# Performance work log

Hardware: AMD Instinct MI355X
Metric: run time of the kernel (lower is better)

## Reference

```python
import jax, jax.numpy as jnp
import numpy as np

K = 50          # NEC paper uses p=50 neighbors
DELTA = 1e-3    # kernel smoothing constant


def setup_inputs() -> dict:
    key = jax.random.key(0)
    ks = jax.random.split(key, 8)
    B, D_IN, D, A, C = 512, 2, 128, 3, 200000
    s = lambda fan_in: 1.0 / np.sqrt(fan_in)
    return {
        "x": jax.random.normal(ks[0], (B, D_IN), jnp.float32),
        "W1": jax.random.normal(ks[1], (D_IN, D), jnp.float32) * s(D_IN),
        "b1": jnp.zeros((D,), jnp.float32),
        "W2": jax.random.normal(ks[2], (D, D), jnp.float32) * s(D),
        "b2": jnp.zeros((D,), jnp.float32),
        "W3": jax.random.normal(ks[3], (D, D), jnp.float32) * s(D),
        "b3": jnp.zeros((D,), jnp.float32),
        "W4": jax.random.normal(ks[4], (D, D), jnp.float32) * s(D),
        "b4": jnp.zeros((D,), jnp.float32),
        "keys": jax.random.normal(ks[5], (A, C, D), jnp.float32),
        "mem_values": jax.random.normal(ks[6], (A, C), jnp.float32),
    }


def _encode(x, W1, b1, W2, b2, W3, b3, W4, b4):
    h = jax.nn.relu(x @ W1 + b1)
    h = jax.nn.relu(h @ W2 + b2)
    h = jax.nn.relu(h @ W3 + b3)
    return h @ W4 + b4  # [B, D]


def _dnd_lookup(h, keys, mem_values):
    # h: [B, D]; keys: [A, C, D]; mem_values: [A, C]
    q2 = jnp.sum(h * h, axis=-1)                       # [B]
    k2 = jnp.sum(keys * keys, axis=-1)                 # [A, C]
    cross = jnp.einsum("bd,acd->bac", h, keys)         # [B, A, C]
    d2 = jnp.maximum(q2[:, None, None] + k2[None] - 2.0 * cross, 0.0)
    neg_d, idx = jax.lax.top_k(-d2, K)                  # [B, A, K]
    d_top = -neg_d
    w = 1.0 / (d_top + DELTA)                           # NEC kernel
    w = w / jnp.sum(w, axis=-1, keepdims=True)
    a_idx = jnp.arange(keys.shape[0])[None, :, None]    # [1, A, 1]
    v_top = mem_values[a_idx, idx]                      # gather -> [B, A, K]
    values = jnp.sum(w * v_top, axis=-1)                # [B, A]
    return values


def reference(x, W1, b1, W2, b2, W3, b3, W4, b4, keys, mem_values):
    h = _encode(x, W1, b1, W2, b2, W3, b3, W4, b4)
    values = _dnd_lookup(h, keys, mem_values)
    actions = jnp.argmax(values, axis=-1)
    return values, actions
```

## Files before the change

kernel.cpp:

```cpp
#include <hip/hip_runtime.h>
#include <hip/hip_bf16.h>
#include <math.h>

#define B_    512
#define DIM   128
#define A_    3
#define C_    200000
#define K_    50
#define DELTA 1e-3

typedef __attribute__((ext_vector_type(8))) short bf16x8;
typedef __attribute__((ext_vector_type(4))) float f32x4;

#define NBIN_A 128
#define CAP_A  1024
#define ROWCH  12500

#define NBLK4  250
#define GT4    32
#define GTPB4  25

#define AOFF_H64   0u
#define AOFF_H32   524288u
#define AOFF_HBF   786432u
#define AOFF_Q2    917504u
#define AOFF_V64   1718272u
#define AOFF_BINS  8022016u
#define NEED_A     (8022016ull + 307200000ull)

#define NBIN_B 192
#define CAP_B  768
#define BM_B   64
#define BN_B   128
#define TPC_B  16
#define CHUNK_B (TPC_B*BN_B)
#define NCH_B  ((C_ + CHUNK_B - 1)/CHUNK_B)

#define BOFF_H32   0u
#define BOFF_H64   262144u
#define BOFF_Q2    786432u
#define BOFF_K2    788480u
#define BOFF_HIST  3188480u
#define BOFF_TAU   4368128u
#define BOFF_CNT   4374272u
#define BOFF_V64   4380416u
#define BOFF_CAND  4392704u

static __device__ inline unsigned short f2bf(float x) {
    union { float f; unsigned u; } c; c.f = x;
    unsigned r = (c.u + 0x7FFFu + ((c.u >> 16) & 1u)) >> 16;
    return (unsigned short)r;
}
static __device__ inline unsigned pkbf(float a, float b) {
    __hip_bfloat162 t = __float22bfloat162_rn(make_float2(a, b));
    union { __hip_bfloat162 h; unsigned u; } cv; cv.h = t; return cv.u;
}

__global__ __launch_bounds__(128) void mlp_kernel(
    const float* __restrict__ x,
    const float* __restrict__ W1, const float* __restrict__ b1,
    const float* __restrict__ W2, const float* __restrict__ b2,
    const float* __restrict__ W3, const float* __restrict__ b3,
    const float* __restrict__ W4, const float* __restrict__ b4,
    float* __restrict__ h32, unsigned short* __restrict__ hbf,
    double* __restrict__ h64, float* __restrict__ q2)
{
    int b = blockIdx.x, t = threadIdx.x;
    __shared__ double s0[DIM], s1[DIM];
    double x0 = (double)x[b*2+0], x1 = (double)x[b*2+1];
    double h = x0*(double)W1[t] + x1*(double)W1[DIM+t] + (double)b1[t];
    s0[t] = h > 0.0 ? h : 0.0;
    __syncthreads();
    double acc = (double)b2[t];
    for (int k = 0; k < DIM; k++) acc += s0[k]*(double)W2[k*DIM+t];
    s1[t] = acc > 0.0 ? acc : 0.0;
    __syncthreads();
    acc = (double)b3[t];
    for (int k = 0; k < DIM; k++) acc += s1[k]*(double)W3[k*DIM+t];
    s0[t] = acc > 0.0 ? acc : 0.0;
    __syncthreads();
    acc = (double)b4[t];
    for (int k = 0; k < DIM; k++) acc += s0[k]*(double)W4[k*DIM+t];
    h64[b*DIM+t] = acc;
    float hf = (float)acc;
    h32[b*DIM+t] = hf;
    hbf[b*DIM+t] = f2bf(hf);
    s1[t] = acc*acc;
    __syncthreads();
    for (int s = 64; s > 0; s >>= 1) { if (t < s) s1[t] += s1[t+s]; __syncthreads(); }
    if (t == 0) q2[b] = (float)s1[0];
}

static __device__ inline void load2(float4 lv[2], const float* __restrict__ ka,
                                    int nrow, int hh) {
    const float4* gp = (const float4*)(ka + (size_t)nrow*DIM) + hh*2;
    lv[0] = gp[0]; lv[1] = gp[1];
}
static __device__ inline void conv_store32(const float4 lv[2], char* sBn,
                                           float* k2n, int r, int hh) {
    float4 v0 = lv[0], v1 = lv[1];
    float ss = v0.x*v0.x + v0.y*v0.y + v0.z*v0.z + v0.w*v0.w
             + v1.x*v1.x + v1.y*v1.y + v1.z*v1.z + v1.w*v1.w;
    int4 pk;
    pk.x = (int)pkbf(v0.x, v0.y); pk.y = (int)pkbf(v0.z, v0.w);
    pk.z = (int)pkbf(v1.x, v1.y); pk.w = (int)pkbf(v1.z, v1.w);
    *(int4*)(sBn + r*256 + ((hh ^ (r & 7)) << 4)) = pk;
    ss += __shfl_xor(ss, 1, 64);
    ss += __shfl_xor(ss, 2, 64);
    ss += __shfl_xor(ss, 4, 64);
    ss += __shfl_xor(ss, 8, 64);
    if (hh == 0) k2n[r] = ss;
}

__global__ __launch_bounds__(512, 1) void gemm4_kernel(
    const float* __restrict__ keys, const unsigned short* __restrict__ hbf,
    const float* __restrict__ q2, unsigned char* __restrict__ bins)
{
    const int blk = blockIdx.x, a = blockIdx.y;
    const int tid = threadIdx.x;
    const int lane = tid & 63, w = tid >> 6;
    const int lm = lane & 15, kh = lane >> 4;

    __shared__ __align__(16) short sA[512*128];
    __shared__ __align__(16) short sB[2][32*128];
    __shared__ float q2s[512];
    __shared__ float k2s[2][32];

    #pragma unroll
    for (int u = 0; u < 16; u++) {
        int idx = u*512 + tid;
        int rr = idx >> 4, cc = idx & 15;
        int4 gv = ((const int4*)hbf)[rr*16 + cc];
        *(int4*)((char*)sA + rr*256 + ((cc ^ (rr & 7)) << 4)) = gv;
    }
    q2s[tid] = q2[tid];

    const int r = tid >> 4, hh = tid & 15;
    const float* ka = keys + (size_t)a*C_*DIM;
    const int nbase = blk*(GT4*GTPB4);

    float4 lv[2];
    load2(lv, ka, nbase + r, hh);
    conv_store32(lv, (char*)&sB[0][0], k2s[0], r, hh);
    __syncthreads();

    unsigned char* rp0; unsigned char* rp1; unsigned char* rp2; unsigned char* rp3;
    {
        unsigned char* base = bins + (size_t)(a*B_)*C_ + kh*4;
        rp0 = base + (size_t)(w*64 +  0 + lm)*C_;
        rp1 = base + (size_t)(w*64 + 16 + lm)*C_;
        rp2 = base + (size_t)(w*64 + 32 + lm)*C_;
        rp3 = base + (size_t)(w*64 + 48 + lm)*C_;
    }

    unsigned pkp[8];
    #pragma unroll
    for (int u = 0; u < 8; u++) pkp[u] = 0;
    int n0_prev = 0;

    int cur = 0;
    for (int t = 0; t < GTPB4; t++) {
        const int n0 = nbase + t*GT4;
        const bool more = (t + 1 < GTPB4);

        if (more) load2(lv, ka, n0 + GT4 + r, hh);
        if (t > 0) {
            *(unsigned*)(rp0 + n0_prev     ) = pkp[0];
            *(unsigned*)(rp0 + n0_prev + 16) = pkp[1];
            *(unsigned*)(rp1 + n0_prev     ) = pkp[2];
            *(unsigned*)(rp1 + n0_prev + 16) = pkp[3];
            *(unsigned*)(rp2 + n0_prev     ) = pkp[4];
            *(unsigned*)(rp2 + n0_prev + 16) = pkp[5];
            *(unsigned*)(rp3 + n0_prev     ) = pkp[6];
            *(unsigned*)(rp3 + n0_prev + 16) = pkp[7];
        }

        f32x4 acc[2][4];
        #pragma unroll
        for (int i = 0; i < 2; i++)
            #pragma unroll
            for (int j = 0; j < 4; j++) acc[i][j] = (f32x4){0.f, 0.f, 0.f, 0.f};

        const char* sBc = (const char*)&sB[cur][0];
        #pragma unroll
        for (int kst = 0; kst < 4; kst++) {
            bf16x8 af[2], bfv[4];
            #pragma unroll
            for (int i = 0; i < 2; i++) {
                int nr = i*16 + lm;
                af[i] = *(const bf16x8*)(sBc + nr*256 + ((((kst<<2) + kh) ^ (nr & 7)) << 4));
            }
            #pragma unroll
            for (int j = 0; j < 4; j++) {
                int br = w*64 + j*16 + lm;
                bfv[j] = *(const bf16x8*)((const char*)sA + br*256 + ((((kst<<2) + kh) ^ (br & 7)) << 4));
            }
            #pragma unroll
            for (int i = 0; i < 2; i++)
                #pragma unroll
                for (int j = 0; j < 4; j++)
                    acc[i][j] = __builtin_amdgcn_mfma_f32_16x16x32_bf16(af[i], bfv[j], acc[i][j], 0, 0, 0);
        }

        {
            float4 kq0 = *(const float4*)&k2s[cur][kh*4];
            float4 kq1 = *(const float4*)&k2s[cur][16 + kh*4];
            #pragma unroll
            for (int j = 0; j < 4; j++) {
                float q2v = q2s[w*64 + j*16 + lm];
                #pragma unroll
                for (int i = 0; i < 2; i++) {
                    float4 kq = (i == 0) ? kq0 : kq1;
                    unsigned pk = 0;
                    #pragma unroll
                    for (int rg = 0; rg < 4; rg++) {
                        float kv = (rg == 0) ? kq.x : (rg == 1) ? kq.y : (rg == 2) ? kq.z : kq.w;
                        float d2v = (q2v + kv) - 2.0f*acc[i][j][rg];
                        float dc = fminf(fmaxf(d2v, 16.0f), 4095.0f);
                        unsigned bin = (__float_as_uint(dc) >> 19) - 2096u;
                        pk |= bin << (8*rg);
                    }
                    pkp[j*2 + i] = pk;
                }
            }
            n0_prev = n0;
        }

        if (more) conv_store32(lv, (char*)&sB[cur ^ 1][0], k2s[cur ^ 1], r, hh);
        __syncthreads();
        cur ^= 1;
    }
    *(unsigned*)(rp0 + n0_prev     ) = pkp[0];
    *(unsigned*)(rp0 + n0_prev + 16) = pkp[1];
    *(unsigned*)(rp1 + n0_prev     ) = pkp[2];
    *(unsigned*)(rp1 + n0_prev + 16) = pkp[3];
    *(unsigned*)(rp2 + n0_prev     ) = pkp[4];
    *(unsigned*)(rp2 + n0_prev + 16) = pkp[5];
    *(unsigned*)(rp3 + n0_prev     ) = pkp[6];
    *(unsigned*)(rp3 + n0_prev + 16) = pkp[7];
}

__global__ __launch_bounds__(512) void finish_kernel(
    const unsigned char* __restrict__ bins, const float* __restrict__ keys,
    const double* __restrict__ h64, const float* __restrict__ mem_values,
    float* __restrict__ out_values, double* __restrict__ val64)
{
    const int q = blockIdx.x;
    const int a = q >> 9, b = q & 511;
    const int p = b*A_ + a;
    const int tid = threadIdx.x;

    __shared__ unsigned hist_s[NBIN_A*32];
    __shared__ unsigned hc[NBIN_A];
    __shared__ double hd[DIM];
    __shared__ unsigned char minb[ROWCH + 12];
    __shared__ int    cidx[CAP_A];
    __shared__ double d2s[CAP_A];
    __shared__ float  vs[CAP_A];
    __shared__ double redv[8];
    __shared__ int    redi8[8];
    __shared__ double acc_w, acc_wv;
    __shared__ unsigned cnt_s;
    __shared__ int thr_s;

    for (int i = tid; i < NBIN_A*32; i += 512) hist_s[i] = 0;
    for (int i = tid; i < DIM; i += 512) hd[i] = h64[(size_t)b*DIM + i];
    if (tid == 0) { cnt_s = 0; acc_w = 0.0; acc_wv = 0.0; }
    __syncthreads();

    const uint4* row = (const uint4*)(bins + (size_t)q*C_);
    const int rep = tid & 31;

    auto proc1 = [&](uint4 v, int ch) {
        unsigned d[4] = {v.x, v.y, v.z, v.w};
        unsigned mn = 255u;
        #pragma unroll
        for (int e = 0; e < 4; e++) {
            unsigned x = d[e];
            unsigned b0 =  x        & 127u;
            unsigned b1 = (x >>  8) & 127u;
            unsigned b2 = (x >> 16) & 127u;
            unsigned b3 = (x >> 24) & 127u;
            atomicAdd(&hist_s[b0*32 + rep], 1u);
            atomicAdd(&hist_s[b1*32 + rep], 1u);
            atomicAdd(&hist_s[b2*32 + rep], 1u);
            atomicAdd(&hist_s[b3*32 + rep], 1u);
            unsigned m01 = b0 < b1 ? b0 : b1;
            unsigned m23 = b2 < b3 ? b2 : b3;
            unsigned m = m01 < m23 ? m01 : m23;
            mn = m < mn ? m : mn;
        }
        minb[ch] = (unsigned char)mn;
    };

    {
        uint4 va[4], vb[4];
        #pragma unroll
        for (int u = 0; u < 4; u++) va[u] = row[u*512 + tid];
        #pragma unroll
        for (int g = 0; g < 6; g += 2) {
            #pragma unroll
            for (int u = 0; u < 4; u++) vb[u] = row[((g+1)*4 + u)*512 + tid];
            #pragma unroll
            for (int u = 0; u < 4; u++) proc1(va[u], (g*4 + u)*512 + tid);
            if (g + 2 < 6) {
                #pragma unroll
                for (int u = 0; u < 4; u++) va[u] = row[((g+2)*4 + u)*512 + tid];
            }
            #pragma unroll
            for (int u = 0; u < 4; u++) proc1(vb[u], ((g+1)*4 + u)*512 + tid);
        }
        if (tid < ROWCH - 24*512) {
            int ch = 24*512 + tid;
            proc1(row[ch], ch);
        }
    }
    __syncthreads();
    if (tid < NBIN_A) {
        unsigned s = 0;
        #pragma unroll
        for (int r2 = 0; r2 < 32; r2++) s += hist_s[tid*32 + r2];
        hc[tid] = s;
    }
    __syncthreads();
    if (tid == 0) {
        unsigned cum = 0; int jsel = NBIN_A-1;
        for (int j = 0; j < NBIN_A; j++) { cum += hc[j]; if (cum >= K_) { jsel = j; break; } }
        unsigned c1 = cum + (jsel+1 < NBIN_A ? hc[jsel+1] : 0u);
        unsigned c2 = c1  + (jsel+2 < NBIN_A ? hc[jsel+2] : 0u);
        int jt = (c2 <= 768u) ? jsel+2 : jsel+1;
        if (jt > NBIN_A-1) jt = NBIN_A-1;
        thr_s = jt + 1;
    }
    __syncthreads();
    const unsigned thr  = (unsigned)thr_s;
    const unsigned addv = (128u - thr) * 0x01010101u;
    for (int ch = tid; ch < ROWCH; ch += 512) {
        if ((unsigned)minb[ch] < thr) {
            uint4 v = row[ch];
            unsigned d[4] = {v.x, v.y, v.z, v.w};
            #pragma unroll
            for (int e = 0; e < 4; e++) {
                unsigned m = (d[e] + addv) & 0x80808080u;
                if (m != 0x80808080u) {
                    #pragma unroll
                    for (int by = 0; by < 4; by++) {
                        if (!((m >> (8*by + 7)) & 1u)) {
                            unsigned pos = atomicAdd(&cnt_s, 1u);
                            if (pos < CAP_A) cidx[pos] = ch*16 + e*4 + by;
                        }
                    }
                }
            }
        }
    }
    __syncthreads();
    int n = (int)cnt_s; if (n > CAP_A) n = CAP_A;

    for (int i = tid; i < n; i += 512) {
        int c = cidx[i];
        const float4* kr = (const float4*)(keys + ((size_t)a*C_ + c)*DIM);
        double s0 = 0.0, s1 = 0.0;
        #pragma unroll 4
        for (int kq = 0; kq < 32; kq++) {
            float4 kv = kr[kq];
            double d0 = hd[4*kq+0] - (double)kv.x;
            double d1 = hd[4*kq+1] - (double)kv.y;
            double d2 = hd[4*kq+2] - (double)kv.z;
            double d3 = hd[4*kq+3] - (double)kv.w;
            s0 += d0*d0 + d1*d1; s1 += d2*d2 + d3*d3;
        }
        d2s[i] = s0 + s1;
        vs[i]  = mem_values[(size_t)a*C_ + c];
    }
    __syncthreads();

    int kk = n < K_ ? n : K_;
    for (int t = 0; t < kk; t++) {
        double best = 1e300; int bi = -1;
        for (int i = tid; i < n; i += 512)
            if (d2s[i] < best) { best = d2s[i]; bi = i; }
        #pragma unroll
        for (int off = 32; off > 0; off >>= 1) {
            double ov = __shfl_xor(best, off, 64);
            int    oi = __shfl_xor(bi,   off, 64);
            if (ov < best) { best = ov; bi = oi; }
        }
        int wv = tid >> 6;
        if ((tid & 63) == 0) { redv[wv] = best; redi8[wv] = bi; }
        __syncthreads();
        if (tid == 0) {
            double bv = redv[0]; int wi = redi8[0];
            #pragma unroll
            for (int u = 1; u < 8; u++)
                if (redv[u] < bv) { bv = redv[u]; wi = redi8[u]; }
            double d = d2s[wi]; if (d < 0.0) d = 0.0;
            double wgt = 1.0 / (d + DELTA);
            acc_w += wgt; acc_wv += wgt * (double)vs[wi];
            d2s[wi] = 2e300;
        }
        __syncthreads();
    }
    if (tid == 0) {
        double v = acc_wv / acc_w;
        out_values[p] = (float)v;
        val64[p] = v;
    }
}

__global__ __launch_bounds__(256) void k2_kernel(const float* __restrict__ keys,
                                                 float* __restrict__ k2)
{
    int r = blockIdx.x*4 + (threadIdx.x >> 6);
    int lane = threadIdx.x & 63;
    float2 v = ((const float2*)keys)[(size_t)r*64 + lane];
    float s = v.x*v.x + v.y*v.y;
    #pragma unroll
    for (int off = 32; off > 0; off >>= 1) s += __shfl_down(s, off, 64);
    if (lane == 0) k2[r] = s;
}

template<int MODE>
__global__ __launch_bounds__(256) void pass_kernel(
    const float* __restrict__ keys, const float* __restrict__ h32,
    const float* __restrict__ q2,   const float* __restrict__ k2,
    unsigned* __restrict__ hist,    const float* __restrict__ tau,
    unsigned* __restrict__ cnt,     int* __restrict__ cand)
{
    const int bt = blockIdx.x;
    const int ch = blockIdx.y;
    const int a  = blockIdx.z;
    const int b0 = bt*BM_B;
    const int tid = threadIdx.x;
    const int tx = tid & 31, ty = tid >> 5;

    __shared__ float4 hs4[BM_B*33];
    __shared__ float4 ks4[BN_B*33];
    __shared__ float  q2s[BM_B];
    __shared__ float  taus[BM_B];
    __shared__ unsigned hist_s[MODE == 0 ? BM_B*NBIN_B : 1];

    #pragma unroll
    for (int q = 0; q < BM_B*32/256; q++) {
        int flat = q*256 + tid; int row = flat >> 5, kq = flat & 31;
        hs4[row*33 + kq] = ((const float4*)h32)[(size_t)(b0+row)*32 + kq];
    }
    if (tid < BM_B) {
        q2s[tid] = q2[b0+tid];
        if (MODE == 1) taus[tid] = tau[(b0+tid)*A_ + a];
    }
    if (MODE == 0) for (int i = tid; i < BM_B*NBIN_B; i += 256) hist_s[i] = 0;
    const float* __restrict__ k2g = k2 + (size_t)a*C_;

    for (int t = 0; t < TPC_B; t++) {
        int n0 = ch*CHUNK_B + t*BN_B;
        if (n0 >= C_) break;
        __syncthreads();
        #pragma unroll
        for (int q = 0; q < 16; q++) {
            int flat = q*256 + tid; int row = flat >> 5, kq = flat & 31;
            int nr = n0 + row; if (nr >= C_) nr = C_-1;
            ks4[row*33 + kq] = ((const float4*)keys)[((size_t)a*C_ + nr)*32 + kq];
        }
        __syncthreads();

        float acc[8][4];
        #pragma unroll
        for (int i = 0; i < 8; i++)
            #pragma unroll
            for (int j = 0; j < 4; j++) acc[i][j] = 0.0f;

        for (int kq = 0; kq < 32; kq++) {
            float4 hv[8], kv[4];
            #pragma unroll
            for (int i = 0; i < 8; i++) hv[i] = hs4[(ty*8+i)*33 + kq];
            #pragma unroll
            for (int j = 0; j < 4; j++) kv[j] = ks4[(j*32+tx)*33 + kq];
            #pragma unroll
            for (int i = 0; i < 8; i++)
                #pragma unroll
                for (int j = 0; j < 4; j++)
                    acc[i][j] += hv[i].x*kv[j].x + hv[i].y*kv[j].y
                               + hv[i].z*kv[j].z + hv[i].w*kv[j].w;
        }

        #pragma unroll
        for (int i = 0; i < 8; i++) {
            int bl = ty*8 + i;
            float q2b = q2s[bl];
            #pragma unroll
            for (int j = 0; j < 4; j++) {
                int n = n0 + j*32 + tx;
                if (n < C_) {
                    float d2f = fmaxf(q2b + k2g[n] - 2.0f*acc[i][j], 0.0f);
                    if (MODE == 0) {
                        int bin = (int)(__float_as_uint(d2f + 1.0f) >> 19) - 2032;
                        bin = bin < 0 ? 0 : (bin > NBIN_B-1 ? NBIN_B-1 : bin);
                        atomicAdd(&hist_s[bl*NBIN_B + bin], 1u);
                    } else {
                        if (d2f < taus[bl]) {
                            int p = (b0+bl)*A_ + a;
                            unsigned pos = atomicAdd(&cnt[p], 1u);
                            if (pos < CAP_B) cand[(size_t)p*CAP_B + pos] = n;
                        }
                    }
                }
            }
        }
    }
    if (MODE == 0) {
        __syncthreads();
        for (int i = tid; i < BM_B*NBIN_B; i += 256) {
            unsigned v = hist_s[i];
            if (v) {
                int bl = i / NBIN_B, bin = i % NBIN_B;
                atomicAdd(&hist[(size_t)((b0+bl)*A_ + a)*NBIN_B + bin], v);
            }
        }
    }
}

__global__ __launch_bounds__(256) void tauB_kernel(const unsigned* __restrict__ hist,
                                                   float* __restrict__ tau)
{
    int p = blockIdx.x*256 + threadIdx.x;
    if (p >= B_*A_) return;
    const unsigned* hp = hist + (size_t)p*NBIN_B;
    unsigned cum = 0; int jsel = NBIN_B-1;
    for (int j = 0; j < NBIN_B; j++) { cum += hp[j]; if (cum >= K_) { jsel = j; break; } }
    tau[p] = __uint_as_float((unsigned)(2034 + jsel) << 19) - 1.0f;
}

__global__ __launch_bounds__(256) void select_kernel(
    const float* __restrict__ keys, const double* __restrict__ h64,
    const float* __restrict__ mem_values,
    const unsigned* __restrict__ cnt, const int* __restrict__ cand,
    float* __restrict__ out_values, double* __restrict__ val64, int cap)
{
    int p = blockIdx.x; int b = p / A_, a = p % A_;
    int tid = threadIdx.x;
    __shared__ double hd[DIM];
    __shared__ double d2s[CAP_A];
    __shared__ float  vs[CAP_A];
    __shared__ double redv[4];
    __shared__ int    redi4[4];
    __shared__ double acc_w, acc_wv;

    for (int i = tid; i < DIM; i += 256) hd[i] = h64[(size_t)b*DIM + i];
    if (tid == 0) { acc_w = 0.0; acc_wv = 0.0; }
    __syncthreads();

    int n = (int)cnt[p]; if (n > cap) n = cap;
    for (int i = tid; i < n; i += 256) {
        int c = cand[(size_t)p*cap + i];
        const float4* kr = (const float4*)(keys + ((size_t)a*C_ + c)*DIM);
        double s0 = 0.0, s1 = 0.0;
        #pragma unroll 4
        for (int kq = 0; kq < 32; kq++) {
            float4 kv = kr[kq];
            double d0 = hd[4*kq+0] - (double)kv.x;
            double d1 = hd[4*kq+1] - (double)kv.y;
            double d2 = hd[4*kq+2] - (double)kv.z;
            double d3 = hd[4*kq+3] - (double)kv.w;
            s0 += d0*d0 + d1*d1; s1 += d2*d2 + d3*d3;
        }
        d2s[i] = s0 + s1;
        vs[i]  = mem_values[(size_t)a*C_ + c];
    }
    __syncthreads();

    int kk = n < K_ ? n : K_;
    for (int t = 0; t < kk; t++) {
        double best = 1e300; int bi = -1;
        for (int i = tid; i < n; i += 256)
            if (d2s[i] < best) { best = d2s[i]; bi = i; }
        #pragma unroll
        for (int off = 32; off > 0; off >>= 1) {
            double ov = __shfl_xor(best, off, 64);
            int    oi = __shfl_xor(bi,   off, 64);
            if (ov < best) { best = ov; bi = oi; }
        }
        int wv = tid >> 6;
        if ((tid & 63) == 0) { redv[wv] = best; redi4[wv] = bi; }
        __syncthreads();
        if (tid == 0) {
            double bv = redv[0]; int wi = redi4[0];
            if (redv[1] < bv) { bv = redv[1]; wi = redi4[1]; }
            if (redv[2] < bv) { bv = redv[2]; wi = redi4[2]; }
            if (redv[3] < bv) { bv = redv[3]; wi = redi4[3]; }
            double d = d2s[wi]; if (d < 0.0) d = 0.0;
            double wgt = 1.0 / (d + DELTA);
            acc_w += wgt; acc_wv += wgt * (double)vs[wi];
            d2s[wi] = 2e300;
        }
        __syncthreads();
    }
    if (tid == 0) {
        double v = acc_wv / acc_w;
        out_values[p] = (float)v;
        val64[p] = v;
    }
}

__global__ void argmax_kernel(const double* __restrict__ val64, float* __restrict__ out)
{
    int b = blockIdx.x*blockDim.x + threadIdx.x;
    if (b >= B_) return;
    double v0 = val64[b*A_+0], v1 = val64[b*A_+1], v2 = val64[b*A_+2];
    int bi = 0; double bv = v0;
    if (v1 > bv) { bv = v1; bi = 1; }
    if (v2 > bv) { bv = v2; bi = 2; }
    out[B_*A_ + b] = (float)bi;
}

extern "C" void kernel_launch(void* const* d_in, const int* in_sizes, int n_in,
                              void* d_out, int out_size, void* d_ws, size_t ws_size,
                              hipStream_t stream)
{
    const float* x    = (const float*)d_in[0];
    const float* W1   = (const float*)d_in[1];
    const float* b1   = (const float*)d_in[2];
    const float* W2   = (const float*)d_in[3];
    const float* b2   = (const float*)d_in[4];
    const float* W3   = (const float*)d_in[5];
    const float* b3   = (const float*)d_in[6];
    const float* W4   = (const float*)d_in[7];
    const float* b4   = (const float*)d_in[8];
    const float* keys = (const float*)d_in[9];
    const float* memv = (const float*)d_in[10];

    char* ws = (char*)d_ws;

    if (ws_size >= NEED_A) {
        double*         h64  = (double*)        (ws + AOFF_H64);
        float*          h32  = (float*)         (ws + AOFF_H32);
        unsigned short* hbf  = (unsigned short*)(ws + AOFF_HBF);
        float*          q2   = (float*)         (ws + AOFF_Q2);
        double*         v64  = (double*)        (ws + AOFF_V64);
        unsigned char*  bins = (unsigned char*) (ws + AOFF_BINS);

        mlp_kernel<<<B_, 128, 0, stream>>>(x, W1, b1, W2, b2, W3, b3, W4, b4, h32, hbf, h64, q2);
        gemm4_kernel<<<dim3(NBLK4, A_), 512, 0, stream>>>(keys, hbf, q2, bins);
        finish_kernel<<<B_*A_, 512, 0, stream>>>(bins, keys, h64, memv, (float*)d_out, v64);
        argmax_kernel<<<2, 256, 0, stream>>>(v64, (float*)d_out);
    } else {
        float*          h32  = (float*)         (ws + BOFF_H32);
        double*         h64  = (double*)        (ws + BOFF_H64);
        float*          q2   = (float*)         (ws + BOFF_Q2);
        float*          k2   = (float*)         (ws + BOFF_K2);
        unsigned*       hist = (unsigned*)      (ws + BOFF_HIST);
        float*          tau  = (float*)         (ws + BOFF_TAU);
        unsigned*       cnt  = (unsigned*)      (ws + BOFF_CNT);
        double*         v64  = (double*)        (ws + BOFF_V64);
        int*            cand = (int*)           (ws + BOFF_CAND);
        unsigned short* hbf  = (unsigned short*)(ws + BOFF_CAND);

        hipMemsetAsync(ws + BOFF_HIST, 0, (BOFF_CNT + B_*A_*4) - BOFF_HIST, stream);

        mlp_kernel<<<B_, 128, 0, stream>>>(x, W1, b1, W2, b2, W3, b3, W4, b4, h32, hbf, h64, q2);
        k2_kernel<<<(A_*C_)/4, 256, 0, stream>>>(keys, k2);
        pass_kernel<0><<<dim3(B_/BM_B, NCH_B, A_), 256, 0, stream>>>(keys, h32, q2, k2, hist, nullptr, nullptr, nullptr);
        tauB_kernel<<<(B_*A_ + 255)/256, 256, 0, stream>>>(hist, tau);
        pass_kernel<1><<<dim3(B_/BM_B, NCH_B, A_), 256, 0, stream>>>(keys, h32, q2, k2, nullptr, tau, cnt, cand);
        select_kernel<<<B_*A_, 256, 0, stream>>>(keys, h64, memv, cnt, cand, (float*)d_out, v64, CAP_B);
        argmax_kernel<<<2, 256, 0, stream>>>(v64, (float*)d_out);
    }
}
```

Measured before the change: 946.3 us.

## Hold query fragments in registers and stream keys directly without LDS staging

The distance-binning GEMM stops staging the 512x128 bf16 query matrix and the key tiles in shared memory. Each wave now keeps its 64 query rows as MFMA fragments in registers. Each wave loads its own 16-key groups straight from global memory, double-buffered in registers, and computes key norms with wave shuffles, which removes all __syncthreads and LDS traffic. This raises register pressure and has every wave re-read the same keys from global/L2 (8 waves per block), in exchange for two blocks per CU and no barriers.

```diff
diff --git a/kernel.cpp b/kernel.cpp
--- a/kernel.cpp
+++ b/kernel.cpp
@@ -16,9 +16,8 @@
 #define CAP_A  1024
 #define ROWCH  12500
 
-#define NBLK4  250
-#define GT4    32
-#define GTPB4  25
+#define NBLK5  250
+#define GPB5   50
 
 #define AOFF_H64   0u
 #define AOFF_H32   524288u
@@ -91,28 +90,15 @@
     if (t == 0) q2[b] = (float)s1[0];
 }
 
-static __device__ inline void load2(float4 lv[2], const float* __restrict__ ka,
-                                    int nrow, int hh) {
-    const float4* gp = (const float4*)(ka + (size_t)nrow*DIM) + hh*2;
-    lv[0] = gp[0]; lv[1] = gp[1];
-}
-static __device__ inline void conv_store32(const float4 lv[2], char* sBn,
-                                           float* k2n, int r, int hh) {
-    float4 v0 = lv[0], v1 = lv[1];
-    float ss = v0.x*v0.x + v0.y*v0.y + v0.z*v0.z + v0.w*v0.w
-             + v1.x*v1.x + v1.y*v1.y + v1.z*v1.z + v1.w*v1.w;
-    int4 pk;
-    pk.x = (int)pkbf(v0.x, v0.y); pk.y = (int)pkbf(v0.z, v0.w);
-    pk.z = (int)pkbf(v1.x, v1.y); pk.w = (int)pkbf(v1.z, v1.w);
-    *(int4*)(sBn + r*256 + ((hh ^ (r & 7)) << 4)) = pk;
-    ss += __shfl_xor(ss, 1, 64);
-    ss += __shfl_xor(ss, 2, 64);
-    ss += __shfl_xor(ss, 4, 64);
-    ss += __shfl_xor(ss, 8, 64);
-    if (hh == 0) k2n[r] = ss;
-}
-
-__global__ __launch_bounds__(512, 1) void gemm4_kernel(
+static __device__ inline void loadg(float4 (&bf)[8], const float* __restrict__ kp) {
+    #pragma unroll
+    for (int kst = 0; kst < 4; kst++) {
+        bf[2*kst]   = *(const float4*)(kp + kst*32);
+        bf[2*kst+1] = *(const float4*)(kp + kst*32 + 4);
+    }
+}
+
+__global__ __launch_bounds__(512, 2) void gemm5_kernel(
     const float* __restrict__ keys, const unsigned short* __restrict__ hbf,
     const float* __restrict__ q2, unsigned char* __restrict__ bins)
 {
@@ -121,123 +107,83 @@
     const int lane = tid & 63, w = tid >> 6;
     const int lm = lane & 15, kh = lane >> 4;
 
-    __shared__ __align__(16) short sA[512*128];
-    __shared__ __align__(16) short sB[2][32*128];
-    __shared__ float q2s[512];
-    __shared__ float k2s[2][32];
-
-    #pragma unroll
-    for (int u = 0; u < 16; u++) {
-        int idx = u*512 + tid;
-        int rr = idx >> 4, cc = idx & 15;
-        int4 gv = ((const int4*)hbf)[rr*16 + cc];
-        *(int4*)((char*)sA + rr*256 + ((cc ^ (rr & 7)) << 4)) = gv;
-    }
-    q2s[tid] = q2[tid];
-
-    const int r = tid >> 4, hh = tid & 15;
-    const float* ka = keys + (size_t)a*C_*DIM;
-    const int nbase = blk*(GT4*GTPB4);
-
-    float4 lv[2];
-    load2(lv, ka, nbase + r, hh);
-    conv_store32(lv, (char*)&sB[0][0], k2s[0], r, hh);
-    __syncthreads();
-
-    unsigned char* rp0; unsigned char* rp1; unsigned char* rp2; unsigned char* rp3;
+    bf16x8 hf[4][4];
+    float q2v[4];
+    unsigned char* bp0; unsigned char* bp1; unsigned char* bp2; unsigned char* bp3;
     {
         unsigned char* base = bins + (size_t)(a*B_)*C_ + kh*4;
-        rp0 = base + (size_t)(w*64 +  0 + lm)*C_;
-        rp1 = base + (size_t)(w*64 + 16 + lm)*C_;
-        rp2 = base + (size_t)(w*64 + 32 + lm)*C_;
-        rp3 = base + (size_t)(w*64 + 48 + lm)*C_;
-    }
-
-    unsigned pkp[8];
+        bp0 = base + (size_t)(w*64 +  0 + lm)*C_;
+        bp1 = base + (size_t)(w*64 + 16 + lm)*C_;
+        bp2 = base + (size_t)(w*64 + 32 + lm)*C_;
+        bp3 = base + (size_t)(w*64 + 48 + lm)*C_;
+    }
     #pragma unroll
-    for (int u = 0; u < 8; u++) pkp[u] = 0;
-    int n0_prev = 0;
-
-    int cur = 0;
-    for (int t = 0; t < GTPB4; t++) {
-        const int n0 = nbase + t*GT4;
-        const bool more = (t + 1 < GTPB4);
-
-        if (more) load2(lv, ka, n0 + GT4 + r, hh);
-        if (t > 0) {
-            *(unsigned*)(rp0 + n0_prev     ) = pkp[0];
-            *(unsigned*)(rp0 + n0_prev + 16) = pkp[1];
-            *(unsigned*)(rp1 + n0_prev     ) = pkp[2];
-            *(unsigned*)(rp1 + n0_prev + 16) = pkp[3];
-            *(unsigned*)(rp2 + n0_prev     ) = pkp[4];
-            *(unsigned*)(rp2 + n0_prev + 16) = pkp[5];
-            *(unsigned*)(rp3 + n0_prev     ) = pkp[6];
-            *(unsigned*)(rp3 + n0_prev + 16) = pkp[7];
-        }
-
-        f32x4 acc[2][4];
-        #pragma unroll
-        for (int i = 0; i < 2; i++)
-            #pragma unroll
-            for (int j = 0; j < 4; j++) acc[i][j] = (f32x4){0.f, 0.f, 0.f, 0.f};
-
-        const char* sBc = (const char*)&sB[cur][0];
+    for (int j = 0; j < 4; j++) {
+        const unsigned short* hp = hbf + (size_t)(w*64 + j*16 + lm)*DIM + kh*8;
+        #pragma unroll
+        for (int kst = 0; kst < 4; kst++)
+            hf[j][kst] = *(const bf16x8*)(hp + kst*32);
+        q2v[j] = q2[w*64 + j*16 + lm];
+    }
+
+    const int nbase = blk*(GPB5*16);
+    const float* __restrict__ kbase =
+        keys + (size_t)a*C_*DIM + ((size_t)nbase + lm)*DIM + kh*8;
+
+    auto process = [&](const float4 (&bf)[8], int g) {
+        const int n0 = nbase + g*16;
+        bf16x8 af[4];
+        float ss = 0.f;
         #pragma unroll
         for (int kst = 0; kst < 4; kst++) {
-            bf16x8 af[2], bfv[4];
-            #pragma unroll
-            for (int i = 0; i < 2; i++) {
-                int nr = i*16 + lm;
-                af[i] = *(const bf16x8*)(sBc + nr*256 + ((((kst<<2) + kh) ^ (nr & 7)) << 4));
+            float4 v0 = bf[2*kst], v1 = bf[2*kst+1];
+            ss += v0.x*v0.x + v0.y*v0.y + v0.z*v0.z + v0.w*v0.w
+                + v1.x*v1.x + v1.y*v1.y + v1.z*v1.z + v1.w*v1.w;
+            union { bf16x8 h; unsigned u[4]; } cv;
+            cv.u[0] = pkbf(v0.x, v0.y);
+            cv.u[1] = pkbf(v0.z, v0.w);
+            cv.u[2] = pkbf(v1.x, v1.y);
+            cv.u[3] = pkbf(v1.z, v1.w);
+            af[kst] = cv.h;
+        }
+        ss += __shfl_xor(ss, 16, 64);
+        ss += __shfl_xor(ss, 32, 64);
+        float kk[4];
+        #pragma unroll
+        for (int r = 0; r < 4; r++) kk[r] = __shfl(ss, kh*4 + r, 64);
+
+        f32x4 acc[4];
+        #pragma unroll
+        for (int j = 0; j < 4; j++) acc[j] = (f32x4){0.f, 0.f, 0.f, 0.f};
+        #pragma unroll
+        for (int kst = 0; kst < 4; kst++)
+            #pragma unroll
+            for (int j = 0; j < 4; j++)
+                acc[j] = __builtin_amdgcn_mfma_f32_16x16x32_bf16(af[kst], hf[j][kst], acc[j], 0, 0, 0);
+
+        #pragma unroll
+        for (int j = 0; j < 4; j++) {
+            unsigned pk = 0;
+            #pragma unroll
+            for (int r = 0; r < 4; r++) {
+                float d2v = (q2v[j] + kk[r]) - 2.0f*acc[j][r];
+                float dc = fminf(fmaxf(d2v, 16.0f), 4095.0f);
+                unsigned bin = (__float_as_uint(dc) >> 19) - 2096u;
+                pk |= bin << (8*r);
             }
-            #pragma unroll
-            for (int j = 0; j < 4; j++) {
-                int br = w*64 + j*16 + lm;
-                bfv[j] = *(const bf16x8*)((const char*)sA + br*256 + ((((kst<<2) + kh) ^ (br & 7)) << 4));
-            }
-            #pragma unroll
-            for (int i = 0; i < 2; i++)
-                #pragma unroll
-                for (int j = 0; j < 4; j++)
-                    acc[i][j] = __builtin_amdgcn_mfma_f32_16x16x32_bf16(af[i], bfv[j], acc[i][j], 0, 0, 0);
-        }
-
-        {
-            float4 kq0 = *(const float4*)&k2s[cur][kh*4];
-            float4 kq1 = *(const float4*)&k2s[cur][16 + kh*4];
-            #pragma unroll
-            for (int j = 0; j < 4; j++) {
-                float q2v = q2s[w*64 + j*16 + lm];
-                #pragma unroll
-                for (int i = 0; i < 2; i++) {
-                    float4 kq = (i == 0) ? kq0 : kq1;
-                    unsigned pk = 0;
-                    #pragma unroll
-                    for (int rg = 0; rg < 4; rg++) {
-                        float kv = (rg == 0) ? kq.x : (rg == 1) ? kq.y : (rg == 2) ? kq.z : kq.w;
-                        float d2v = (q2v + kv) - 2.0f*acc[i][j][rg];
-                        float dc = fminf(fmaxf(d2v, 16.0f), 4095.0f);
-                        unsigned bin = (__float_as_uint(dc) >> 19) - 2096u;
-                        pk |= bin << (8*rg);
-                    }
-                    pkp[j*2 + i] = pk;
-                }
-            }
-            n0_prev = n0;
-        }
-
-        if (more) conv_store32(lv, (char*)&sB[cur ^ 1][0], k2s[cur ^ 1], r, hh);
-        __syncthreads();
-        cur ^= 1;
-    }
-    *(unsigned*)(rp0 + n0_prev     ) = pkp[0];
-    *(unsigned*)(rp0 + n0_prev + 16) = pkp[1];
-    *(unsigned*)(rp1 + n0_prev     ) = pkp[2];
-    *(unsigned*)(rp1 + n0_prev + 16) = pkp[3];
-    *(unsigned*)(rp2 + n0_prev     ) = pkp[4];
-    *(unsigned*)(rp2 + n0_prev + 16) = pkp[5];
-    *(unsigned*)(rp3 + n0_prev     ) = pkp[6];
-    *(unsigned*)(rp3 + n0_prev + 16) = pkp[7];
+            unsigned char* bp = (j==0)?bp0:(j==1)?bp1:(j==2)?bp2:bp3;
+            *(unsigned*)(bp + n0) = pk;
+        }
+    };
+
+    float4 bufA[8], bufB[8];
+    loadg(bufA, kbase);
+    for (int g = 0; g < GPB5; g += 2) {
+        if (g + 1 < GPB5) loadg(bufB, kbase + (size_t)(g+1)*16*DIM);
+        process(bufA, g);
+        if (g + 2 < GPB5) loadg(bufA, kbase + (size_t)(g+2)*16*DIM);
+        if (g + 1 < GPB5) process(bufB, g + 1);
+    }
 }
 
 __global__ __launch_bounds__(512) void finish_kernel(
@@ -640,7 +586,7 @@
         unsigned char*  bins = (unsigned char*) (ws + AOFF_BINS);
 
         mlp_kernel<<<B_, 128, 0, stream>>>(x, W1, b1, W2, b2, W3, b3, W4, b4, h32, hbf, h64, q2);
-        gemm4_kernel<<<dim3(NBLK4, A_), 512, 0, stream>>>(keys, hbf, q2, bins);
+        gemm5_kernel<<<dim3(NBLK5, A_), 512, 0, stream>>>(keys, hbf, q2, bins);
         finish_kernel<<<B_*A_, 512, 0, stream>>>(bins, keys, h64, memv, (float*)d_out, v64);
         argmax_kernel<<<2, 256, 0, stream>>>(v64, (float*)d_out);
     } else {
```

After: 1.141 ms. 1.21x slower.

## Build histogram from per-chunk minimum bins, then rescan only candidate chunks

Applied to the files above, without the earlier changes.

The first pass now makes one shared-memory atomic per 16-element chunk, keyed on the chunk's minimum bin, in place of sixteen per-element atomics. A coarse window bound is taken from that chunk-min histogram. Chunks whose minimum is within the window are reloaded from global memory to build the exact per-element histogram. This cuts LDS atomic traffic but adds a second pass with extra barriers and reloads of the candidate chunks. The chunk-min histogram only approximates the element histogram, so the window depends on the chunk-min distribution.

```diff
diff --git a/kernel.cpp b/kernel.cpp
--- a/kernel.cpp
+++ b/kernel.cpp
@@ -261,7 +261,7 @@
     __shared__ int    redi8[8];
     __shared__ double acc_w, acc_wv;
     __shared__ unsigned cnt_s;
-    __shared__ int thr_s;
+    __shared__ int thr_s, W_s;
 
     for (int i = tid; i < NBIN_A*32; i += 512) hist_s[i] = 0;
     for (int i = tid; i < DIM; i += 512) hd[i] = h64[(size_t)b*DIM + i];
@@ -281,16 +281,13 @@
             unsigned b1 = (x >>  8) & 127u;
             unsigned b2 = (x >> 16) & 127u;
             unsigned b3 = (x >> 24) & 127u;
-            atomicAdd(&hist_s[b0*32 + rep], 1u);
-            atomicAdd(&hist_s[b1*32 + rep], 1u);
-            atomicAdd(&hist_s[b2*32 + rep], 1u);
-            atomicAdd(&hist_s[b3*32 + rep], 1u);
             unsigned m01 = b0 < b1 ? b0 : b1;
             unsigned m23 = b2 < b3 ? b2 : b3;
             unsigned m = m01 < m23 ? m01 : m23;
             mn = m < mn ? m : mn;
         }
         minb[ch] = (unsigned char)mn;
+        atomicAdd(&hist_s[mn*32 + rep], 1u);
     };
 
     {
@@ -313,6 +310,40 @@
         if (tid < ROWCH - 24*512) {
             int ch = 24*512 + tid;
             proc1(row[ch], ch);
+        }
+    }
+    __syncthreads();
+    if (tid < NBIN_A) {
+        unsigned s = 0;
+        #pragma unroll
+        for (int r2 = 0; r2 < 32; r2++) s += hist_s[tid*32 + r2];
+        hc[tid] = s;
+    }
+    __syncthreads();
+    if (tid == 0) {
+        unsigned cum = 0; int jhi = NBIN_A-1;
+        for (int j = 0; j < NBIN_A; j++) { cum += hc[j]; if (cum >= K_) { jhi = j; break; } }
+        int Wv = jhi + 2; if (Wv > NBIN_A-1) Wv = NBIN_A-1;
+        W_s = Wv;
+    }
+    __syncthreads();
+    const int W = W_s;
+
+    for (int i = tid; i < NBIN_A*32; i += 512) hist_s[i] = 0;
+    __syncthreads();
+
+    for (int ch = tid; ch < ROWCH; ch += 512) {
+        if ((int)minb[ch] <= W) {
+            uint4 v = row[ch];
+            unsigned d[4] = {v.x, v.y, v.z, v.w};
+            #pragma unroll
+            for (int e = 0; e < 4; e++) {
+                unsigned x = d[e];
+                atomicAdd(&hist_s[((x      ) & 127u)*32 + rep], 1u);
+                atomicAdd(&hist_s[((x >>  8) & 127u)*32 + rep], 1u);
+                atomicAdd(&hist_s[((x >> 16) & 127u)*32 + rep], 1u);
+                atomicAdd(&hist_s[((x >> 24) & 127u)*32 + rep], 1u);
+            }
         }
     }
     __syncthreads();
```

Measured after the change: 976.0 us. +3.1%, slower.
